# Optimization experiments

Measured on AMD Instinct MI355X. Metric: run time of the kernel, lower is better.

## Reference

```python
import jax, jax.numpy as jnp
import numpy as np
from jax import lax

H_IMG, W_IMG = 1280, 1280
STRIDES = (8, 16, 32, 64, 128)
FEAT_SHAPES = tuple((H_IMG // s) * (W_IMG // s) for s in STRIDES)  # (25600,6400,1600,400,100)
N_POINTS = sum(FEAT_SHAPES)  # 34100
NUM_CLASSES = 1
TOPK = 1000
SCORE_THRESH = 0.05
NMS_THRESH = 0.5
MAX_DET = 300
BATCH = 8
N_GT = 200


def make_points():
    # matches AnchorFreePS.reference_points: cell centers at stride*i + stride//2, (cx, cy) order
    pts = []
    for s in STRIDES:
        h, w = H_IMG // s, W_IMG // s
        cx = np.arange(w, dtype=np.float32) * s + s // 2
        cy = np.arange(h, dtype=np.float32) * s + s // 2
        gy, gx = np.meshgrid(cy, cx, indexing='ij')
        pts.append(np.stack([gx, gy], axis=-1).reshape(-1, 2))
    return jnp.asarray(np.concatenate(pts, axis=0))


def setup_inputs() -> dict:
    key = jax.random.key(0)
    k1, k2, k3, k4 = jax.random.split(key, 4)
    points = make_points()  # [N,2]
    xy = jax.random.uniform(k1, (BATCH, N_GT, 2), minval=0.0, maxval=1000.0)
    wh = jax.random.uniform(k2, (BATCH, N_GT, 2), minval=20.0, maxval=260.0)
    gt_boxes = jnp.concatenate([xy, xy + wh], axis=-1)  # [B,M,4] x1y1x2y2
    cls_logits = jax.random.normal(k3, (BATCH, N_POINTS, NUM_CLASSES)) * 1.5 - 3.0
    regression = jax.random.uniform(k4, (BATCH, N_POINTS, 4)) * 0.1  # normalized ltrb codes
    return {"points": points, "gt_boxes": gt_boxes, "cls_logits": cls_logits, "regression": regression}


def match_points_to_boxes(points, gt_boxes):
    # point-in-box test + area-cost argmin (compute_loss matched_idxs)
    px = points[None, :, None, 0]  # [1,N,1]
    py = points[None, :, None, 1]
    b = gt_boxes[:, None, :, :]    # [B,1,M,4]
    inside = (px >= b[..., 0]) & (px <= b[..., 2]) & (py >= b[..., 1]) & (py <= b[..., 3])  # [B,N,M]
    matched = jnp.any(inside, axis=-1)  # [B,N]
    areas = (gt_boxes[..., 2] - gt_boxes[..., 0]) * (gt_boxes[..., 3] - gt_boxes[..., 1])  # [B,M]
    BIG = jnp.float32(2 ** 31 - 1)  # torch.iinfo(torch.int).max
    cost = jnp.where(inside, areas[:, None, :], BIG)
    idx = jnp.argmin(cost, axis=-1)
    return jnp.where(matched, idx, -1)


def decode_boxes(rel, pts):
    # FCOSBoxCoder.decode_single with weights (1,1,1,1)
    l = rel[:, 0] * W_IMG
    t = rel[:, 1] * H_IMG
    r = rel[:, 2] * W_IMG
    b = rel[:, 3] * H_IMG
    x, y = pts[:, 0], pts[:, 1]
    return jnp.stack([x - l, y - t, x + r, y + b], axis=-1)


def clip_boxes(boxes):
    return jnp.stack([
        jnp.clip(boxes[:, 0], 0.0, W_IMG),
        jnp.clip(boxes[:, 1], 0.0, H_IMG),
        jnp.clip(boxes[:, 2], 0.0, W_IMG),
        jnp.clip(boxes[:, 3], 0.0, H_IMG)], axis=-1)


def nms(boxes, scores, labels, valid_init):
    # fixed-size sequential NMS equivalent to batched_nms (same-label suppression)
    work = lax.stop_gradient(jnp.where(valid_init, scores, -jnp.inf))

    def body(w, _):
        i = jnp.argmax(w)
        s = w[i]
        box = boxes[i]
        x1 = jnp.maximum(box[0], boxes[:, 0])
        y1 = jnp.maximum(box[1], boxes[:, 1])
        x2 = jnp.minimum(box[2], boxes[:, 2])
        y2 = jnp.minimum(box[3], boxes[:, 3])
        inter = jnp.clip(x2 - x1, 0.0) * jnp.clip(y2 - y1, 0.0)
        a1 = (box[2] - box[0]) * (box[3] - box[1])
        a2 = (boxes[:, 2] - boxes[:, 0]) * (boxes[:, 3] - boxes[:, 1])
        iou = inter / (a1 + a2 - inter + 1e-9)
        supp = (iou > NMS_THRESH) & (labels == labels[i])
        w = jnp.where(supp, -jnp.inf, w).at[i].set(-jnp.inf)
        return w, (i, s)

    _, (idxs, picked) = lax.scan(body, work, None, length=MAX_DET)
    valid = picked > -jnp.inf
    return idxs, valid


def postprocess_image(points, cls_i, reg_i):
    bx_list, sc_list, lb_list = [], [], []
    off = 0
    for size in FEAT_SHAPES:  # fixed small level loop
        sl = slice(off, off + size)
        off += size
        scores = jax.nn.sigmoid(cls_i[sl]).reshape(-1)  # [size*C]
        k = min(TOPK, size * NUM_CLASSES)
        sc, idx = lax.top_k(scores, k)
        a = idx // NUM_CLASSES
        lb = idx % NUM_CLASSES
        bx = clip_boxes(decode_boxes(reg_i[sl][a], points[sl][a]))
        bx_list.append(bx)
        sc_list.append(sc)
        lb_list.append(lb)
    boxes = jnp.concatenate(bx_list, axis=0)
    scores = jnp.concatenate(sc_list, axis=0)
    labels = jnp.concatenate(lb_list, axis=0)
    idxs, valid = nms(boxes, scores, labels, scores > SCORE_THRESH)
    out_boxes = jnp.where(valid[:, None], boxes[idxs], 0.0)
    out_scores = jnp.where(valid, scores[idxs], 0.0)
    out_labels = jnp.where(valid, labels[idxs], -1)
    return out_boxes, out_scores, out_labels, valid


def reference(points, gt_boxes, cls_logits, regression):
    matched_idxs = match_points_to_boxes(points, gt_boxes)  # [B,N]
    boxes, scores, labels, valid = jax.vmap(
        lambda c, r: postprocess_image(points, c, r))(cls_logits, regression)
    return matched_idxs, boxes, scores, labels, valid
```

## Files before the change

kernel.cpp:

```cpp
#include <hip/hip_runtime.h>
#include <stdint.h>

#define N_POINTS   34100
#define BATCH      8
#define N_GT       200
#define NLEV       5
#define NCAND      3500
#define MAX_DET    300
#define SCORE_TH   0.05f
#define NMS_TH     0.5f
#define IMG        1280.0f
#define NBIN       4096
#define TIE_CAP    4096
#define MTH 0.50000002980232238769531250

#define OUT_MATCH  0
#define OUT_BOXES  272800
#define OUT_SCORES 282400
#define OUT_LABELS 284800
#define OUT_VALID  287200

#define WS_KEYS    0
#define WS_PARAMS  1746560
#define WS_SBOX    2632192
#define WS_SSC     3080192
#define WS_MASK    3192192
#define WS_DIAG    9500032
#define MASK_STRIDE 98560
#define DIAG_STRIDE 3520

typedef unsigned long long u64;
typedef uint32_t u32;

__device__ __forceinline__ int mask_off(int c) {
    int g = c >> 6;
    return 64 * (55 * g - (g * (g - 1)) / 2) + (c - (g << 6)) * (55 - g);
}

__device__ __forceinline__ int level_of(int p) {
    return (p < 25600) ? 0 : (p < 32000) ? 1 : (p < 33600) ? 2 : (p < 34000) ? 3 : 4;
}
__device__ __forceinline__ int loff_of(int l) {
    return (l == 0) ? 0 : (l == 1) ? 25600 : (l == 2) ? 32000 : (l == 3) ? 33600 : 34000;
}
__device__ __forceinline__ int lsize_of(int l) {
    return (l == 0) ? 25600 : (l == 1) ? 6400 : (l == 2) ? 1600 : (l == 3) ? 400 : 100;
}
__device__ __forceinline__ int k_of(int l) {
    return (l == 0) ? 1000 : (l == 1) ? 1000 : (l == 2) ? 1000 : (l == 3) ? 400 : 100;
}
__device__ __forceinline__ u64 readlane64(u64 v, int t) {
    u32 lo = (u32)__builtin_amdgcn_readlane((int)(u32)v, t);
    u32 hi = (u32)__builtin_amdgcn_readlane((int)(u32)(v >> 32), t);
    return ((u64)hi << 32) | lo;
}

#define MPT 2
__global__ __launch_bounds__(256)
void match_key_kernel(const float* __restrict__ points,
                      const float* __restrict__ gt,
                      const float* __restrict__ logits,
                      float* __restrict__ out_match,
                      u32* __restrict__ keys) {
#pragma clang fp contract(off)
    __shared__ float bx1[N_GT], by1[N_GT], bx2[N_GT], by2[N_GT], ar[N_GT];
    const int b = blockIdx.y;
    const int base = blockIdx.x * (256 * MPT) + threadIdx.x;

    for (int j = threadIdx.x; j < N_GT; j += 256) {
        float x1 = gt[(b * N_GT + j) * 4 + 0];
        float y1 = gt[(b * N_GT + j) * 4 + 1];
        float x2 = gt[(b * N_GT + j) * 4 + 2];
        float y2 = gt[(b * N_GT + j) * 4 + 3];
        bx1[j] = x1; by1[j] = y1; bx2[j] = x2; by2[j] = y2;
        ar[j] = (x2 - x1) * (y2 - y1);
    }
    __syncthreads();

    const float BIGF = 2147483648.0f;
    float px[MPT], py[MPT], best[MPT];
    int bi[MPT];
#pragma unroll
    for (int k = 0; k < MPT; ++k) {
        int p = base + k * 256;
        int pc = (p < N_POINTS) ? p : 0;
        px[k] = points[pc * 2 + 0];
        py[k] = points[pc * 2 + 1];
        best[k] = BIGF; bi[k] = -1;
    }
    for (int j = 0; j < N_GT; ++j) {
        float x1 = bx1[j], y1 = by1[j], x2 = bx2[j], y2 = by2[j], a = ar[j];
#pragma unroll
        for (int k = 0; k < MPT; ++k) {
            bool inside = (px[k] >= x1) && (px[k] <= x2) &&
                          (py[k] >= y1) && (py[k] <= y2);
            float cost = inside ? a : BIGF;
            if (cost < best[k]) { best[k] = cost; bi[k] = j; }
        }
    }
#pragma unroll
    for (int k = 0; k < MPT; ++k) {
        int p = base + k * 256;
        if (p >= N_POINTS) continue;
        out_match[b * N_POINTS + p] = (float)bi[k];
        float lg = logits[b * N_POINTS + p];
        float s = 1.0f / (1.0f + expf(-lg));
        u32 u = __float_as_uint(s);
        u32 key = (u & 0x80000000u) ? ~u : (u | 0x80000000u);
        keys[b * N_POINTS + p] = key;
    }
}

__global__ __launch_bounds__(256)
void hist_select_kernel(const u32* __restrict__ keys,
                        u32* __restrict__ params) {
    __shared__ u32 h[NBIN];
    const int seg = blockIdx.x;
    const int b = seg / NLEV;
    const int l = seg - b * NLEV;
    const int tid = threadIdx.x;

    for (int i = tid; i < NBIN; i += 256) h[i] = 0u;
    __syncthreads();

    const u32* k = keys + b * N_POINTS + loff_of(l);
    const int n = lsize_of(l);
    for (int i = tid; i < n; i += 256)
        atomicAdd(&h[(k[i] >> 19) & 4095u], 1u);
    __syncthreads();

    if (tid < 64) {
        const u32 K = (u32)k_of(l);
        const int lane = tid;
        u32 S = 0;
#pragma unroll 8
        for (int i = 0; i < 64; ++i) S += h[lane * 64 + i];
        u32 acc = S;
#pragma unroll
        for (int off = 1; off < 64; off <<= 1) {
            u32 v = (u32)__shfl_down((int)acc, off);
            if (lane + off < 64) acc += v;
        }
        u32 sfxAfter = acc - S;
        bool hit = (sfxAfter < K) && (sfxAfter + S >= K);
        u64 bal = __ballot(hit);
        int Lg = (int)__builtin_ctzll(bal);
        u32 sfxG = (u32)__shfl((int)sfxAfter, Lg);

        u32 v = h[Lg * 64 + lane];
        u32 acc2 = v;
#pragma unroll
        for (int off = 1; off < 64; off <<= 1) {
            u32 t = (u32)__shfl_down((int)acc2, off);
            if (lane + off < 64) acc2 += t;
        }
        u32 sfx2 = sfxG + acc2 - v;
        bool hit2 = (sfx2 < K) && (sfx2 + v >= K);
        if (hit2) {
            params[seg * 2 + 0] = (u32)(Lg * 64 + lane);
            params[seg * 2 + 1] = K - sfx2;
        }
    }
}

#define SORT_T 1024
__global__ __launch_bounds__(SORT_T)
void pipeline_kernel(const u32* __restrict__ keys,
                     const u32* __restrict__ params,
                     const float* __restrict__ reg,
                     const float* __restrict__ points,
                     float* __restrict__ sboxes,
                     float* __restrict__ sscores) {
#pragma clang fp contract(off)
    __shared__ u64 sk[4096];
    __shared__ u64 tb[TIE_CAP];
    __shared__ u64 aux[4096];
    __shared__ u32 h[NBIN];
    __shared__ u32 bs[NBIN];
    __shared__ u32 sTl[NLEV], skkl[NLEV], wt[16];
    __shared__ u32 scnt, stcnt;

    const int b = blockIdx.x;
    const int tid = threadIdx.x;
    const int lane = tid & 63;
    const int wid = tid >> 6;
    const u32* kk_ = keys + b * N_POINTS;

    if (tid < NLEV) {
        sTl[tid]  = params[(b * NLEV + tid) * 2 + 0];
        skkl[tid] = params[(b * NLEV + tid) * 2 + 1];
    }
    if (tid == 0) { scnt = 0u; stcnt = 0u; }
    __syncthreads();

    const int NPAIR = N_POINTS / 2;
    for (int i0 = tid; i0 - tid < NPAIR; i0 += SORT_T) {
        bool act = i0 < NPAIR;
        int p0 = act ? (2 * i0) : 0;
        int p1 = p0 + 1;
        u32 key0 = kk_[p0], key1 = kk_[p1];
        int l0 = level_of(p0), l1 = level_of(p1);
        u32 d0 = (key0 >> 19) & 4095u, d1 = (key1 >> 19) & 4095u;
        u32 T0 = sTl[l0], T1 = sTl[l1];
        bool def0 = act && (d0 > T0), def1 = act && (d1 > T1);
        bool tie0 = act && (d0 == T0), tie1 = act && (d1 == T1);
        u64 k0 = ((u64)key0 << 18) | ((u64)(7 - l0) << 15)
               | (u64)(32767 - (p0 - loff_of(l0)));
        u64 k1 = ((u64)key1 << 18) | ((u64)(7 - l1) << 15)
               | (u64)(32767 - (p1 - loff_of(l1)));

        u32 nd = (u32)def0 + (u32)def1;
        u32 pre = nd;
#pragma unroll
        for (int off = 1; off < 64; off <<= 1) {
            u32 v = (u32)__shfl_up((int)pre, off);
            if (lane >= off) pre += v;
        }
        u32 base_ = 0;
        if (lane == 63 && pre) base_ = atomicAdd(&scnt, pre);
        base_ = (u32)__shfl((int)base_, 63);
        u32 ex = pre - nd;
        if (def0) sk[base_ + ex] = k0;
        if (def1) sk[base_ + ex + (u32)def0] = k1;

        u32 nt = (u32)tie0 + (u32)tie1;
        u32 pret = nt;
#pragma unroll
        for (int off = 1; off < 64; off <<= 1) {
            u32 v = (u32)__shfl_up((int)pret, off);
            if (lane >= off) pret += v;
        }
        u32 baset = 0;
        if (lane == 63 && pret) baset = atomicAdd(&stcnt, pret);
        baset = (u32)__shfl((int)baset, 63);
        u32 ext = pret - nt;
        if (tie0 && baset + ext < TIE_CAP) tb[baset + ext] = k0;
        if (tie1 && baset + ext + (u32)tie0 < TIE_CAP)
            tb[baset + ext + (u32)tie0] = k1;
    }
    __syncthreads();

    const u64 below = (lane == 0) ? 0ull : (~0ull >> (64 - lane));
    int t = (int)stcnt; if (t > TIE_CAP) t = TIE_CAP;
    for (int j0 = tid; j0 - tid < t; j0 += SORT_T) {
        bool active = j0 < t;
        u64 kj = active ? tb[j0] : 0ull;
        u32 lvtag = (u32)(kj >> 15) & 7u;
        int r = 0;
        for (int i = 0; i < t; ++i) {
            u64 ki = tb[i];
            r += (ki > kj && (((u32)(ki >> 15) & 7u) == lvtag)) ? 1 : 0;
        }
        bool inc = active && (r < (int)skkl[7 - lvtag]);
        u64 grp = __ballot(inc);
        if (grp) {
            int leader = (int)__builtin_ctzll(grp);
            u32 base_ = 0;
            if (lane == leader)
                base_ = atomicAdd(&scnt, (u32)__builtin_popcountll(grp));
            base_ = (u32)__shfl((int)base_, leader);
            if (inc) sk[base_ + (u32)__builtin_popcountll(grp & below)] = kj;
        }
    }
    __syncthreads();
    const int total = (int)scnt;

    for (int i = tid; i < NBIN; i += SORT_T) h[i] = 0u;
    __syncthreads();
    for (int i = tid; i < total; i += SORT_T)
        atomicAdd(&h[(u32)(sk[i] >> 37) & 4095u], 1u);
    __syncthreads();

    u32 t0 = h[4095 - 4 * tid];
    u32 t1 = h[4095 - (4 * tid + 1)];
    u32 t2 = h[4095 - (4 * tid + 2)];
    u32 t3 = h[4095 - (4 * tid + 3)];
    u32 tsum = t0 + t1 + t2 + t3;
    u32 sc_ = tsum;
#pragma unroll
    for (int off = 1; off < 64; off <<= 1) {
        u32 v = (u32)__shfl_up((int)sc_, off);
        if (lane >= off) sc_ += v;
    }
    if (lane == 63) wt[wid] = sc_;
    __syncthreads();
    if (tid < 64) {
        u32 v = (tid < 16) ? wt[tid] : 0u;
        u32 s2 = v;
#pragma unroll
        for (int off = 1; off < 16; off <<= 1) {
            u32 x = (u32)__shfl_up((int)s2, off);
            if (tid >= off) s2 += x;
        }
        if (tid < 16) wt[tid] = s2 - v;
    }
    __syncthreads();
    u32 run = (sc_ - tsum) + wt[wid];
    bs[4095 - 4 * tid] = run;       run += t0;
    bs[4095 - (4 * tid + 1)] = run; run += t1;
    bs[4095 - (4 * tid + 2)] = run; run += t2;
    bs[4095 - (4 * tid + 3)] = run;
    __syncthreads();
    for (int i = tid; i < NBIN; i += SORT_T) h[i] = 0u;
    __syncthreads();
    for (int i = tid; i < total; i += SORT_T) {
        u64 k = sk[i];
        u32 d = (u32)(k >> 37) & 4095u;
        u32 pos = bs[d] + atomicAdd(&h[d], 1u);
        aux[pos] = k;
    }
    __syncthreads();
    for (int p = tid; p < total; p += SORT_T) {
        u64 kp = aux[p];
        u32 d = (u32)(kp >> 37) & 4095u;
        u32 gbase = bs[d];
        u32 gend = (d == 0) ? (u32)total : bs[d - 1];
        u32 r = 0;
        for (u32 q = gbase; q < gend; ++q) r += (aux[q] > kp) ? 1u : 0u;
        sk[gbase + r] = kp;
    }
    __syncthreads();

    for (int r = tid; r < NCAND; r += SORT_T) {
        float x1 = 0.f, y1 = 0.f, x2 = 0.f, y2 = 0.f, sc = 0.f;
        if (r < total) {
            u64 k50 = sk[r];
            int lowb = (int)(k50 & 0x3FFFFull);
            int l = 7 - (lowb >> 15);
            int idxl = 32767 - (lowb & 32767);
            int p = loff_of(l) + idxl;
            u32 key32 = (u32)(k50 >> 18);
            sc = __uint_as_float(key32 ^ 0x80000000u);
            int gp = b * N_POINTS + p;
            float l_ = reg[gp * 4 + 0] * IMG;
            float t_ = reg[gp * 4 + 1] * IMG;
            float r_ = reg[gp * 4 + 2] * IMG;
            float bb = reg[gp * 4 + 3] * IMG;
            float px = points[p * 2 + 0];
            float py = points[p * 2 + 1];
            x1 = fminf(fmaxf(px - l_, 0.0f), IMG);
            y1 = fminf(fmaxf(py - t_, 0.0f), IMG);
            x2 = fminf(fmaxf(px + r_, 0.0f), IMG);
            y2 = fminf(fmaxf(py + bb, 0.0f), IMG);
        }
        int slot = b * NCAND + r;
        sboxes[slot * 4 + 0] = x1;
        sboxes[slot * 4 + 1] = y1;
        sboxes[slot * 4 + 2] = x2;
        sboxes[slot * 4 + 3] = y2;
        sscores[slot] = sc;
    }
}

__global__ __launch_bounds__(256)
void mask_kernel(const float* __restrict__ sboxes,
                 const float* __restrict__ sscores,
                 u64* __restrict__ mask,
                 u64* __restrict__ diag) {
#pragma clang fp contract(off)
    const int b = blockIdx.y;
    const int wv = threadIdx.x >> 6;
    const int lane = threadIdx.x & 63;
    const int NG = (NCAND + 3) >> 2;
    const int NH = (NG + 1) >> 1;
    const int gidx = blockIdx.x * 4 + wv;
    if (gidx >= NH) return;

    const float4* gb = (const float4*)sboxes + b * NCAND;
    const float* gs = sscores + b * NCAND;
    u64* mout = mask + (size_t)b * MASK_STRIDE;
    u64* dout = diag + (size_t)b * DIAG_STRIDE;

    for (int s = 0; s < 2; ++s) {
        const int g0 = (s == 0) ? gidx : (NG - 1 - gidx);
        if (s == 1 && g0 == gidx) break;
        const int c0 = g0 << 2;

        float4 bc[4]; float a1[4]; bool ok[4]; int g[4]; u64* rp[4];
        bool any = false;
#pragma unroll
        for (int i = 0; i < 4; ++i) {
            int c = c0 + i;
            int cc = (c < NCAND) ? c : (NCAND - 1);
            bc[i] = gb[cc];
            a1[i] = (bc[i].z - bc[i].x) * (bc[i].w - bc[i].y);
            ok[i] = (c < NCAND) && (gs[cc] > SCORE_TH);
            g[i] = cc >> 6;
            rp[i] = mout + mask_off(cc) - g[i];
            any |= ok[i];
        }
        if (!any) continue;

        for (int w = (c0 >> 6); w < 55; ++w) {
            int cj = (w << 6) + lane;
            float4 bj = (cj < NCAND) ? gb[cj] : make_float4(0.f, 0.f, 0.f, 0.f);
            float a2 = (bj.z - bj.x) * (bj.w - bj.y);
#pragma unroll
            for (int i = 0; i < 4; ++i) {
                float x1 = fmaxf(bc[i].x, bj.x);
                float y1 = fmaxf(bc[i].y, bj.y);
                float x2 = fminf(bc[i].z, bj.z);
                float y2 = fminf(bc[i].w, bj.w);
                float inter = fmaxf(x2 - x1, 0.f) * fmaxf(y2 - y1, 0.f);
                float denom = a1[i] + a2 - inter + 1e-9f;
                float hf = 0.5f * denom;
                float rr = fmaf(0x1p-25f, denom, hf);
                u64 bits = __ballot(inter > rr);
                u64 eq = __ballot(inter == rr);
                if (eq) {
                    u64 fb = __ballot((double)inter > MTH * (double)denom);
                    bits |= (eq & fb);
                }
                if (lane == 0 && ok[i] && w >= g[i]) {
                    rp[i][w] = bits;
                    if (w == g[i]) dout[c0 + i] = bits;
                }
            }
        }
    }
}

__global__ __launch_bounds__(64)
void scan_kernel(const float* __restrict__ sboxes,
                 const float* __restrict__ sscores,
                 const u64* __restrict__ mask,
                 const u64* __restrict__ diag,
                 float* __restrict__ out) {
    const int b = blockIdx.x;
    const int lane = threadIdx.x;
    const float4* gb = (const float4*)sboxes + b * NCAND;
    const float* gs = sscores + b * NCAND;
    const u64* mrow = mask + (size_t)b * MASK_STRIDE;
    const u64* drow = diag + (size_t)b * DIAG_STRIDE;

    float* ob = out + OUT_BOXES  + b * MAX_DET * 4;
    float* os = out + OUT_SCORES + b * MAX_DET;
    float* ol = out + OUT_LABELS + b * MAX_DET;
    float* ov = out + OUT_VALID  + b * MAX_DET;

    u64 m = 0ull;
    u64 rowN = drow[lane];
    float4 bjN = gb[lane];
    float sjN = gs[lane];

    int kept = 0;
    for (int w = 0; w < 55; ++w) {
        const int wbase = w << 6;
        const u64 row = rowN;
        const float4 bj = bjN;
        const float sj = sjN;
        if (w < 54) {
            int cn = wbase + 64 + lane;
            int cc = (cn < NCAND) ? cn : (NCAND - 1);
            rowN = drow[cc];
            bjN = gb[cc];
            float s = gs[cc];
            sjN = (cn < NCAND) ? s : 0.f;
        }
        int c = wbase + lane;
        u64 bad = __ballot(!((c < NCAND) && (sj > SCORE_TH)));
        u64 cur = readlane64(m, w) | bad;
        u64 km = 0ull;
        while (kept < MAX_DET) {
            u64 avail = ~cur;
            if (avail == 0ull) break;
            int t = (int)__builtin_ctzll(avail);
            u64 r = readlane64(row, t);
            cur |= r | (1ull << t);
            km |= 1ull << t;
            if (lane == t) {
                ob[kept * 4 + 0] = bj.x;
                ob[kept * 4 + 1] = bj.y;
                ob[kept * 4 + 2] = bj.z;
                ob[kept * 4 + 3] = bj.w;
                os[kept] = sj;
                ol[kept] = 0.0f;
                ov[kept] = 1.0f;
            }
            kept++;
        }
        if (km) {
            const bool lr = (lane >= w && lane < 55);
            const int lo = lane - w;
            u64 acc = 0ull;
            while (km) {
#define POPBIT(tn) int tn = -1; if (km) { tn = (int)__builtin_ctzll(km); km &= km - 1ull; }
                POPBIT(t0) POPBIT(t1) POPBIT(t2) POPBIT(t3)
                POPBIT(t4) POPBIT(t5) POPBIT(t6) POPBIT(t7)
#undef POPBIT
                u64 v0 = 0, v1 = 0, v2 = 0, v3 = 0, v4 = 0, v5 = 0, v6 = 0, v7 = 0;
                if (lr) {
                    v0 = mrow[mask_off(wbase + t0) + lo];
                    if (t1 >= 0) v1 = mrow[mask_off(wbase + t1) + lo];
                    if (t2 >= 0) v2 = mrow[mask_off(wbase + t2) + lo];
                    if (t3 >= 0) v3 = mrow[mask_off(wbase + t3) + lo];
                    if (t4 >= 0) v4 = mrow[mask_off(wbase + t4) + lo];
                    if (t5 >= 0) v5 = mrow[mask_off(wbase + t5) + lo];
                    if (t6 >= 0) v6 = mrow[mask_off(wbase + t6) + lo];
                    if (t7 >= 0) v7 = mrow[mask_off(wbase + t7) + lo];
                }
                acc |= ((v0 | v1) | (v2 | v3)) | ((v4 | v5) | (v6 | v7));
            }
            m |= acc;
        }
        if (kept >= MAX_DET) break;
    }
    for (int k = kept + lane; k < MAX_DET; k += 64) {
        ob[k * 4 + 0] = 0.f; ob[k * 4 + 1] = 0.f;
        ob[k * 4 + 2] = 0.f; ob[k * 4 + 3] = 0.f;
        os[k] = 0.f; ol[k] = -1.f; ov[k] = 0.f;
    }
}

extern "C" void kernel_launch(void* const* d_in, const int* in_sizes, int n_in,
                              void* d_out, int out_size, void* d_ws, size_t ws_size,
                              hipStream_t stream) {
    const float* points = (const float*)d_in[0];
    const float* gt     = (const float*)d_in[1];
    const float* logits = (const float*)d_in[2];
    const float* reg    = (const float*)d_in[3];
    float* out = (float*)d_out;

    u32* keys      = (u32*)((char*)d_ws + WS_KEYS);
    u32* params    = (u32*)((char*)d_ws + WS_PARAMS);
    float* sboxes  = (float*)((char*)d_ws + WS_SBOX);
    float* sscores = (float*)((char*)d_ws + WS_SSC);
    u64* mask   = (u64*)((char*)d_ws + WS_MASK);
    u64* diag   = (u64*)((char*)d_ws + WS_DIAG);

    dim3 g1((N_POINTS + 256 * MPT - 1) / (256 * MPT), BATCH);
    match_key_kernel<<<g1, 256, 0, stream>>>(points, gt, logits,
                                             out + OUT_MATCH, keys);

    hist_select_kernel<<<BATCH * NLEV, 256, 0, stream>>>(keys, params);

    pipeline_kernel<<<BATCH, SORT_T, 0, stream>>>(keys, params, reg, points,
                                                  sboxes, sscores);

    dim3 g5((((NCAND + 3) / 4 + 1) / 2 + 3) / 4, BATCH);
    mask_kernel<<<g5, 256, 0, stream>>>(sboxes, sscores, mask, diag);

    scan_kernel<<<BATCH, 64, 0, stream>>>(sboxes, sscores, mask, diag, out);
}
```

Baseline: 280.6 us.

## Fuse all stages into one cooperative persistent kernel with grid syncs

Merges the five launches (match/keys, histogram select, per-image sort/decode, mask build, NMS scan) into a single cooperative kernel of 256 blocks of 1024 threads, separated by grid-wide syncs. The point-to-box matching now runs on the spare blocks while the 8 per-image sort blocks work, so those two stages overlap. The aim is to remove launch gaps and let the large matching work hide behind the serial per-image sort. In exchange, all stages share one large static shared-memory buffer and 1024-thread blocks, which can lower occupancy. Grid syncs add their own latency, and a cooperative launch needs every block to be resident at once.

```diff
diff --git a/kernel.cpp b/kernel.cpp
--- a/kernel.cpp
+++ b/kernel.cpp
@@ -1,5 +1,8 @@
 #include <hip/hip_runtime.h>
+#include <hip/hip_cooperative_groups.h>
 #include <stdint.h>
+
+namespace cg = cooperative_groups;
 
 #define N_POINTS   34100
 #define BATCH      8
@@ -29,6 +32,9 @@
 #define MASK_STRIDE 98560
 #define DIAG_STRIDE 3520
 
+#define NBLK   256
+#define NTHR   1024
+
 typedef unsigned long long u64;
 typedef uint32_t u32;
 
@@ -36,7 +42,6 @@
     int g = c >> 6;
     return 64 * (55 * g - (g * (g - 1)) / 2) + (c - (g << 6)) * (55 - g);
 }
-
 __device__ __forceinline__ int level_of(int p) {
     return (p < 25600) ? 0 : (p < 32000) ? 1 : (p < 33600) ? 2 : (p < 34000) ? 3 : 4;
 }
@@ -55,460 +60,453 @@
     return ((u64)hi << 32) | lo;
 }
 
-#define MPT 2
-__global__ __launch_bounds__(256)
-void match_key_kernel(const float* __restrict__ points,
-                      const float* __restrict__ gt,
-                      const float* __restrict__ logits,
-                      float* __restrict__ out_match,
-                      u32* __restrict__ keys) {
+__global__ __launch_bounds__(NTHR)
+void mega_kernel(const float* __restrict__ points,
+                 const float* __restrict__ gt,
+                 const float* __restrict__ logits,
+                 const float* __restrict__ reg,
+                 float* __restrict__ out,
+                 u32* __restrict__ keys,
+                 u32* __restrict__ params,
+                 float* __restrict__ sboxes,
+                 float* __restrict__ sscores,
+                 u64* __restrict__ mask,
+                 u64* __restrict__ diag) {
 #pragma clang fp contract(off)
-    __shared__ float bx1[N_GT], by1[N_GT], bx2[N_GT], by2[N_GT], ar[N_GT];
-    const int b = blockIdx.y;
-    const int base = blockIdx.x * (256 * MPT) + threadIdx.x;
-
-    for (int j = threadIdx.x; j < N_GT; j += 256) {
-        float x1 = gt[(b * N_GT + j) * 4 + 0];
-        float y1 = gt[(b * N_GT + j) * 4 + 1];
-        float x2 = gt[(b * N_GT + j) * 4 + 2];
-        float y2 = gt[(b * N_GT + j) * 4 + 3];
-        bx1[j] = x1; by1[j] = y1; bx2[j] = x2; by2[j] = y2;
-        ar[j] = (x2 - x1) * (y2 - y1);
-    }
-    __syncthreads();
-
-    const float BIGF = 2147483648.0f;
-    float px[MPT], py[MPT], best[MPT];
-    int bi[MPT];
-#pragma unroll
-    for (int k = 0; k < MPT; ++k) {
-        int p = base + k * 256;
-        int pc = (p < N_POINTS) ? p : 0;
-        px[k] = points[pc * 2 + 0];
-        py[k] = points[pc * 2 + 1];
-        best[k] = BIGF; bi[k] = -1;
-    }
-    for (int j = 0; j < N_GT; ++j) {
-        float x1 = bx1[j], y1 = by1[j], x2 = bx2[j], y2 = by2[j], a = ar[j];
-#pragma unroll
-        for (int k = 0; k < MPT; ++k) {
-            bool inside = (px[k] >= x1) && (px[k] <= x2) &&
-                          (py[k] >= y1) && (py[k] <= y2);
-            float cost = inside ? a : BIGF;
-            if (cost < best[k]) { best[k] = cost; bi[k] = j; }
-        }
-    }
-#pragma unroll
-    for (int k = 0; k < MPT; ++k) {
-        int p = base + k * 256;
-        if (p >= N_POINTS) continue;
-        out_match[b * N_POINTS + p] = (float)bi[k];
-        float lg = logits[b * N_POINTS + p];
-        float s = 1.0f / (1.0f + expf(-lg));
-        u32 u = __float_as_uint(s);
-        u32 key = (u & 0x80000000u) ? ~u : (u | 0x80000000u);
-        keys[b * N_POINTS + p] = key;
-    }
-}
-
-__global__ __launch_bounds__(256)
-void hist_select_kernel(const u32* __restrict__ keys,
-                        u32* __restrict__ params) {
-    __shared__ u32 h[NBIN];
-    const int seg = blockIdx.x;
-    const int b = seg / NLEV;
-    const int l = seg - b * NLEV;
-    const int tid = threadIdx.x;
-
-    for (int i = tid; i < NBIN; i += 256) h[i] = 0u;
-    __syncthreads();
-
-    const u32* k = keys + b * N_POINTS + loff_of(l);
-    const int n = lsize_of(l);
-    for (int i = tid; i < n; i += 256)
-        atomicAdd(&h[(k[i] >> 19) & 4095u], 1u);
-    __syncthreads();
-
-    if (tid < 64) {
-        const u32 K = (u32)k_of(l);
-        const int lane = tid;
-        u32 S = 0;
-#pragma unroll 8
-        for (int i = 0; i < 64; ++i) S += h[lane * 64 + i];
-        u32 acc = S;
-#pragma unroll
-        for (int off = 1; off < 64; off <<= 1) {
-            u32 v = (u32)__shfl_down((int)acc, off);
-            if (lane + off < 64) acc += v;
-        }
-        u32 sfxAfter = acc - S;
-        bool hit = (sfxAfter < K) && (sfxAfter + S >= K);
-        u64 bal = __ballot(hit);
-        int Lg = (int)__builtin_ctzll(bal);
-        u32 sfxG = (u32)__shfl((int)sfxAfter, Lg);
-
-        u32 v = h[Lg * 64 + lane];
-        u32 acc2 = v;
-#pragma unroll
-        for (int off = 1; off < 64; off <<= 1) {
-            u32 t = (u32)__shfl_down((int)acc2, off);
-            if (lane + off < 64) acc2 += t;
-        }
-        u32 sfx2 = sfxG + acc2 - v;
-        bool hit2 = (sfx2 < K) && (sfx2 + v >= K);
-        if (hit2) {
-            params[seg * 2 + 0] = (u32)(Lg * 64 + lane);
-            params[seg * 2 + 1] = K - sfx2;
-        }
-    }
-}
-
-#define SORT_T 1024
-__global__ __launch_bounds__(SORT_T)
-void pipeline_kernel(const u32* __restrict__ keys,
-                     const u32* __restrict__ params,
-                     const float* __restrict__ reg,
-                     const float* __restrict__ points,
-                     float* __restrict__ sboxes,
-                     float* __restrict__ sscores) {
-#pragma clang fp contract(off)
-    __shared__ u64 sk[4096];
-    __shared__ u64 tb[TIE_CAP];
-    __shared__ u64 aux[4096];
-    __shared__ u32 h[NBIN];
-    __shared__ u32 bs[NBIN];
+    cg::grid_group gg = cg::this_grid();
+    __shared__ __align__(16) char smem[131072];
     __shared__ u32 sTl[NLEV], skkl[NLEV], wt[16];
     __shared__ u32 scnt, stcnt;
 
-    const int b = blockIdx.x;
     const int tid = threadIdx.x;
     const int lane = tid & 63;
     const int wid = tid >> 6;
-    const u32* kk_ = keys + b * N_POINTS;
-
-    if (tid < NLEV) {
-        sTl[tid]  = params[(b * NLEV + tid) * 2 + 0];
-        skkl[tid] = params[(b * NLEV + tid) * 2 + 1];
+    const int blk = blockIdx.x;
+
+    for (int i = blk * NTHR + tid; i < BATCH * N_POINTS; i += NBLK * NTHR) {
+        float lgv = logits[i];
+        float s = 1.0f / (1.0f + expf(-lgv));
+        u32 u = __float_as_uint(s);
+        keys[i] = (u & 0x80000000u) ? ~u : (u | 0x80000000u);
     }
-    if (tid == 0) { scnt = 0u; stcnt = 0u; }
-    __syncthreads();
-
-    const int NPAIR = N_POINTS / 2;
-    for (int i0 = tid; i0 - tid < NPAIR; i0 += SORT_T) {
-        bool act = i0 < NPAIR;
-        int p0 = act ? (2 * i0) : 0;
-        int p1 = p0 + 1;
-        u32 key0 = kk_[p0], key1 = kk_[p1];
-        int l0 = level_of(p0), l1 = level_of(p1);
-        u32 d0 = (key0 >> 19) & 4095u, d1 = (key1 >> 19) & 4095u;
-        u32 T0 = sTl[l0], T1 = sTl[l1];
-        bool def0 = act && (d0 > T0), def1 = act && (d1 > T1);
-        bool tie0 = act && (d0 == T0), tie1 = act && (d1 == T1);
-        u64 k0 = ((u64)key0 << 18) | ((u64)(7 - l0) << 15)
-               | (u64)(32767 - (p0 - loff_of(l0)));
-        u64 k1 = ((u64)key1 << 18) | ((u64)(7 - l1) << 15)
-               | (u64)(32767 - (p1 - loff_of(l1)));
-
-        u32 nd = (u32)def0 + (u32)def1;
-        u32 pre = nd;
+    gg.sync();
+
+    if (blk < BATCH * NLEV) {
+        u32* h2 = (u32*)smem;
+        const int seg = blk;
+        const int b = seg / NLEV;
+        const int l = seg - b * NLEV;
+        for (int i = tid; i < NBIN; i += NTHR) h2[i] = 0u;
+        __syncthreads();
+        const u32* k = keys + b * N_POINTS + loff_of(l);
+        const int n = lsize_of(l);
+        for (int i = tid; i < n; i += NTHR)
+            atomicAdd(&h2[(k[i] >> 19) & 4095u], 1u);
+        __syncthreads();
+        if (tid < 64) {
+            const u32 K = (u32)k_of(l);
+            u32 S = 0;
+#pragma unroll 8
+            for (int i = 0; i < 64; ++i) S += h2[lane * 64 + i];
+            u32 acc = S;
+#pragma unroll
+            for (int off = 1; off < 64; off <<= 1) {
+                u32 v = (u32)__shfl_down((int)acc, off);
+                if (lane + off < 64) acc += v;
+            }
+            u32 sfxAfter = acc - S;
+            bool hit = (sfxAfter < K) && (sfxAfter + S >= K);
+            u64 bal = __ballot(hit);
+            int Lg = (int)__builtin_ctzll(bal);
+            u32 sfxG = (u32)__shfl((int)sfxAfter, Lg);
+            u32 v = h2[Lg * 64 + lane];
+            u32 acc2 = v;
+#pragma unroll
+            for (int off = 1; off < 64; off <<= 1) {
+                u32 t = (u32)__shfl_down((int)acc2, off);
+                if (lane + off < 64) acc2 += t;
+            }
+            u32 sfx2 = sfxG + acc2 - v;
+            bool hit2 = (sfx2 < K) && (sfx2 + v >= K);
+            if (hit2) {
+                params[seg * 2 + 0] = (u32)(Lg * 64 + lane);
+                params[seg * 2 + 1] = K - sfx2;
+            }
+        }
+    }
+    gg.sync();
+
+    if (blk < BATCH) {
+        u64* sk  = (u64*)smem;
+        u64* tb  = (u64*)(smem + 32768);
+        u64* aux = (u64*)(smem + 65536);
+        u32* h   = (u32*)(smem + 98304);
+        u32* bs  = (u32*)(smem + 114688);
+        const int b = blk;
+        const u32* kk_ = keys + b * N_POINTS;
+
+        if (tid < NLEV) {
+            sTl[tid]  = params[(b * NLEV + tid) * 2 + 0];
+            skkl[tid] = params[(b * NLEV + tid) * 2 + 1];
+        }
+        if (tid == 0) { scnt = 0u; stcnt = 0u; }
+        __syncthreads();
+
+        const int NPAIR = N_POINTS / 2;
+        for (int i0 = tid; i0 - tid < NPAIR; i0 += NTHR) {
+            bool act = i0 < NPAIR;
+            int p0 = act ? (2 * i0) : 0;
+            int p1 = p0 + 1;
+            u32 key0 = kk_[p0], key1 = kk_[p1];
+            int l0 = level_of(p0), l1 = level_of(p1);
+            u32 d0 = (key0 >> 19) & 4095u, d1 = (key1 >> 19) & 4095u;
+            u32 T0 = sTl[l0], T1 = sTl[l1];
+            bool def0 = act && (d0 > T0), def1 = act && (d1 > T1);
+            bool tie0 = act && (d0 == T0), tie1 = act && (d1 == T1);
+            u64 k0 = ((u64)key0 << 18) | ((u64)(7 - l0) << 15)
+                   | (u64)(32767 - (p0 - loff_of(l0)));
+            u64 k1 = ((u64)key1 << 18) | ((u64)(7 - l1) << 15)
+                   | (u64)(32767 - (p1 - loff_of(l1)));
+
+            u32 nd = (u32)def0 + (u32)def1;
+            u32 pre = nd;
+#pragma unroll
+            for (int off = 1; off < 64; off <<= 1) {
+                u32 v = (u32)__shfl_up((int)pre, off);
+                if (lane >= off) pre += v;
+            }
+            u32 base_ = 0;
+            if (lane == 63 && pre) base_ = atomicAdd(&scnt, pre);
+            base_ = (u32)__shfl((int)base_, 63);
+            u32 ex = pre - nd;
+            if (def0) sk[base_ + ex] = k0;
+            if (def1) sk[base_ + ex + (u32)def0] = k1;
+
+            u32 nt = (u32)tie0 + (u32)tie1;
+            u32 pret = nt;
+#pragma unroll
+            for (int off = 1; off < 64; off <<= 1) {
+                u32 v = (u32)__shfl_up((int)pret, off);
+                if (lane >= off) pret += v;
+            }
+            u32 baset = 0;
+            if (lane == 63 && pret) baset = atomicAdd(&stcnt, pret);
+            baset = (u32)__shfl((int)baset, 63);
+            u32 ext = pret - nt;
+            if (tie0 && baset + ext < TIE_CAP) tb[baset + ext] = k0;
+            if (tie1 && baset + ext + (u32)tie0 < TIE_CAP)
+                tb[baset + ext + (u32)tie0] = k1;
+        }
+        __syncthreads();
+
+        const u64 below = (lane == 0) ? 0ull : (~0ull >> (64 - lane));
+        int t = (int)stcnt; if (t > TIE_CAP) t = TIE_CAP;
+        for (int j0 = tid; j0 - tid < t; j0 += NTHR) {
+            bool active = j0 < t;
+            u64 kj = active ? tb[j0] : 0ull;
+            u32 lvtag = (u32)(kj >> 15) & 7u;
+            int r = 0;
+            for (int i = 0; i < t; ++i) {
+                u64 ki = tb[i];
+                r += (ki > kj && (((u32)(ki >> 15) & 7u) == lvtag)) ? 1 : 0;
+            }
+            bool inc = active && (r < (int)skkl[7 - lvtag]);
+            u64 grp = __ballot(inc);
+            if (grp) {
+                int leader = (int)__builtin_ctzll(grp);
+                u32 base_ = 0;
+                if (lane == leader)
+                    base_ = atomicAdd(&scnt, (u32)__builtin_popcountll(grp));
+                base_ = (u32)__shfl((int)base_, leader);
+                if (inc) sk[base_ + (u32)__builtin_popcountll(grp & below)] = kj;
+            }
+        }
+        __syncthreads();
+        const int total = (int)scnt;
+
+        for (int i = tid; i < NBIN; i += NTHR) h[i] = 0u;
+        __syncthreads();
+        for (int i = tid; i < total; i += NTHR)
+            atomicAdd(&h[(u32)(sk[i] >> 37) & 4095u], 1u);
+        __syncthreads();
+
+        u32 t0 = h[4095 - 4 * tid];
+        u32 t1 = h[4095 - (4 * tid + 1)];
+        u32 t2 = h[4095 - (4 * tid + 2)];
+        u32 t3 = h[4095 - (4 * tid + 3)];
+        u32 tsum = t0 + t1 + t2 + t3;
+        u32 sc_ = tsum;
 #pragma unroll
         for (int off = 1; off < 64; off <<= 1) {
-            u32 v = (u32)__shfl_up((int)pre, off);
-            if (lane >= off) pre += v;
-        }
-        u32 base_ = 0;
-        if (lane == 63 && pre) base_ = atomicAdd(&scnt, pre);
-        base_ = (u32)__shfl((int)base_, 63);
-        u32 ex = pre - nd;
-        if (def0) sk[base_ + ex] = k0;
-        if (def1) sk[base_ + ex + (u32)def0] = k1;
-
-        u32 nt = (u32)tie0 + (u32)tie1;
-        u32 pret = nt;
-#pragma unroll
-        for (int off = 1; off < 64; off <<= 1) {
-            u32 v = (u32)__shfl_up((int)pret, off);
-            if (lane >= off) pret += v;
-        }
-        u32 baset = 0;
-        if (lane == 63 && pret) baset = atomicAdd(&stcnt, pret);
-        baset = (u32)__shfl((int)baset, 63);
-        u32 ext = pret - nt;
-        if (tie0 && baset + ext < TIE_CAP) tb[baset + ext] = k0;
-        if (tie1 && baset + ext + (u32)tie0 < TIE_CAP)
-            tb[baset + ext + (u32)tie0] = k1;
+            u32 v = (u32)__shfl_up((int)sc_, off);
+            if (lane >= off) sc_ += v;
+        }
+        if (lane == 63) wt[wid] = sc_;
+        __syncthreads();
+        if (tid < 64) {
+            u32 v = (tid < 16) ? wt[tid] : 0u;
+            u32 s2 = v;
+#pragma unroll
+            for (int off = 1; off < 16; off <<= 1) {
+                u32 x = (u32)__shfl_up((int)s2, off);
+                if (tid >= off) s2 += x;
+            }
+            if (tid < 16) wt[tid] = s2 - v;
+        }
+        __syncthreads();
+        u32 run = (sc_ - tsum) + wt[wid];
+        bs[4095 - 4 * tid] = run;       run += t0;
+        bs[4095 - (4 * tid + 1)] = run; run += t1;
+        bs[4095 - (4 * tid + 2)] = run; run += t2;
+        bs[4095 - (4 * tid + 3)] = run;
+        __syncthreads();
+        for (int i = tid; i < NBIN; i += NTHR) h[i] = 0u;
+        __syncthreads();
+        for (int i = tid; i < total; i += NTHR) {
+            u64 k = sk[i];
+            u32 d = (u32)(k >> 37) & 4095u;
+            u32 pos = bs[d] + atomicAdd(&h[d], 1u);
+            aux[pos] = k;
+        }
+        __syncthreads();
+        for (int p = tid; p < total; p += NTHR) {
+            u64 kp = aux[p];
+            u32 d = (u32)(kp >> 37) & 4095u;
+            u32 gbase = bs[d];
+            u32 gend = (d == 0) ? (u32)total : bs[d - 1];
+            u32 r = 0;
+            for (u32 q = gbase; q < gend; ++q) r += (aux[q] > kp) ? 1u : 0u;
+            sk[gbase + r] = kp;
+        }
+        __syncthreads();
+
+        for (int r = tid; r < NCAND; r += NTHR) {
+            float x1 = 0.f, y1 = 0.f, x2 = 0.f, y2 = 0.f, sc = 0.f;
+            if (r < total) {
+                u64 k50 = sk[r];
+                int lowb = (int)(k50 & 0x3FFFFull);
+                int l = 7 - (lowb >> 15);
+                int idxl = 32767 - (lowb & 32767);
+                int p = loff_of(l) + idxl;
+                u32 key32 = (u32)(k50 >> 18);
+                sc = __uint_as_float(key32 ^ 0x80000000u);
+                int gp = b * N_POINTS + p;
+                float l_ = reg[gp * 4 + 0] * IMG;
+                float t_ = reg[gp * 4 + 1] * IMG;
+                float r_ = reg[gp * 4 + 2] * IMG;
+                float bb = reg[gp * 4 + 3] * IMG;
+                float px = points[p * 2 + 0];
+                float py = points[p * 2 + 1];
+                x1 = fminf(fmaxf(px - l_, 0.0f), IMG);
+                y1 = fminf(fmaxf(py - t_, 0.0f), IMG);
+                x2 = fminf(fmaxf(px + r_, 0.0f), IMG);
+                y2 = fminf(fmaxf(py + bb, 0.0f), IMG);
+            }
+            int slot = b * NCAND + r;
+            sboxes[slot * 4 + 0] = x1;
+            sboxes[slot * 4 + 1] = y1;
+            sboxes[slot * 4 + 2] = x2;
+            sboxes[slot * 4 + 3] = y2;
+            sscores[slot] = sc;
+        }
+    } else {
+        float* bx1 = (float*)smem;
+        float* by1 = bx1 + 256;
+        float* bx2 = bx1 + 512;
+        float* by2 = bx1 + 768;
+        float* ar  = bx1 + 1024;
+        const int q = blk - BATCH;
+        const int b = q / 31;
+        const int j = q - b * 31;
+        for (int i = tid; i < N_GT; i += NTHR) {
+            float x1 = gt[(b * N_GT + i) * 4 + 0];
+            float y1 = gt[(b * N_GT + i) * 4 + 1];
+            float x2 = gt[(b * N_GT + i) * 4 + 2];
+            float y2 = gt[(b * N_GT + i) * 4 + 3];
+            bx1[i] = x1; by1[i] = y1; bx2[i] = x2; by2[i] = y2;
+            ar[i] = (x2 - x1) * (y2 - y1);
+        }
+        __syncthreads();
+
+        const float BIGF = 2147483648.0f;
+        const int STR = 31 * NTHR;
+        float px[2], py[2], best[2];
+        int bi[2];
+#pragma unroll
+        for (int k = 0; k < 2; ++k) {
+            int p = j * NTHR + tid + k * STR;
+            int pc = (p < N_POINTS) ? p : 0;
+            px[k] = points[pc * 2 + 0];
+            py[k] = points[pc * 2 + 1];
+            best[k] = BIGF; bi[k] = -1;
+        }
+        for (int i = 0; i < N_GT; ++i) {
+            float x1 = bx1[i], y1 = by1[i], x2 = bx2[i], y2 = by2[i], a = ar[i];
+#pragma unroll
+            for (int k = 0; k < 2; ++k) {
+                bool inside = (px[k] >= x1) && (px[k] <= x2) &&
+                              (py[k] >= y1) && (py[k] <= y2);
+                float cost = inside ? a : BIGF;
+                if (cost < best[k]) { best[k] = cost; bi[k] = i; }
+            }
+        }
+#pragma unroll
+        for (int k = 0; k < 2; ++k) {
+            int p = j * NTHR + tid + k * STR;
+            if (p < N_POINTS)
+                out[OUT_MATCH + b * N_POINTS + p] = (float)bi[k];
+        }
     }
-    __syncthreads();
-
-    const u64 below = (lane == 0) ? 0ull : (~0ull >> (64 - lane));
-    int t = (int)stcnt; if (t > TIE_CAP) t = TIE_CAP;
-    for (int j0 = tid; j0 - tid < t; j0 += SORT_T) {
-        bool active = j0 < t;
-        u64 kj = active ? tb[j0] : 0ull;
-        u32 lvtag = (u32)(kj >> 15) & 7u;
-        int r = 0;
-        for (int i = 0; i < t; ++i) {
-            u64 ki = tb[i];
-            r += (ki > kj && (((u32)(ki >> 15) & 7u) == lvtag)) ? 1 : 0;
-        }
-        bool inc = active && (r < (int)skkl[7 - lvtag]);
-        u64 grp = __ballot(inc);
-        if (grp) {
-            int leader = (int)__builtin_ctzll(grp);
-            u32 base_ = 0;
-            if (lane == leader)
-                base_ = atomicAdd(&scnt, (u32)__builtin_popcountll(grp));
-            base_ = (u32)__shfl((int)base_, leader);
-            if (inc) sk[base_ + (u32)__builtin_popcountll(grp & below)] = kj;
+    gg.sync();
+
+    {
+        const int NG = (NCAND + 3) >> 2;
+        const int NH = (NG + 1) >> 1;
+        const int wg = blk * 16 + wid;
+        if (wg < NH * BATCH) {
+            const int b = wg & 7;
+            const int gidx = wg >> 3;
+            const float4* gb = (const float4*)sboxes + b * NCAND;
+            const float* gs = sscores + b * NCAND;
+            u64* mout = mask + (size_t)b * MASK_STRIDE;
+            u64* dout = diag + (size_t)b * DIAG_STRIDE;
+
+            for (int s = 0; s < 2; ++s) {
+                const int g0 = (s == 0) ? gidx : (NG - 1 - gidx);
+                if (s == 1 && g0 == gidx) break;
+                const int c0 = g0 << 2;
+
+                float4 bc[4]; float a1[4]; bool ok[4]; int g[4]; u64* rp[4];
+                bool any = false;
+#pragma unroll
+                for (int i = 0; i < 4; ++i) {
+                    int c = c0 + i;
+                    int cc = (c < NCAND) ? c : (NCAND - 1);
+                    bc[i] = gb[cc];
+                    a1[i] = (bc[i].z - bc[i].x) * (bc[i].w - bc[i].y);
+                    ok[i] = (c < NCAND) && (gs[cc] > SCORE_TH);
+                    g[i] = cc >> 6;
+                    rp[i] = mout + mask_off(cc) - g[i];
+                    any |= ok[i];
+                }
+                if (!any) continue;
+
+                for (int w = (c0 >> 6); w < 55; ++w) {
+                    int cj = (w << 6) + lane;
+                    float4 bj = (cj < NCAND) ? gb[cj]
+                                             : make_float4(0.f, 0.f, 0.f, 0.f);
+                    float a2 = (bj.z - bj.x) * (bj.w - bj.y);
+#pragma unroll
+                    for (int i = 0; i < 4; ++i) {
+                        float x1 = fmaxf(bc[i].x, bj.x);
+                        float y1 = fmaxf(bc[i].y, bj.y);
+                        float x2 = fminf(bc[i].z, bj.z);
+                        float y2 = fminf(bc[i].w, bj.w);
+                        float inter = fmaxf(x2 - x1, 0.f) * fmaxf(y2 - y1, 0.f);
+                        float denom = a1[i] + a2 - inter + 1e-9f;
+                        float hf = 0.5f * denom;
+                        float rr = fmaf(0x1p-25f, denom, hf);
+                        u64 bits = __ballot(inter > rr);
+                        u64 eq = __ballot(inter == rr);
+                        if (eq) {
+                            u64 fb = __ballot((double)inter > MTH * (double)denom);
+                            bits |= (eq & fb);
+                        }
+                        if (lane == 0 && ok[i] && w >= g[i]) {
+                            rp[i][w] = bits;
+                            if (w == g[i]) dout[c0 + i] = bits;
+                        }
+                    }
+                }
+            }
         }
     }
-    __syncthreads();
-    const int total = (int)scnt;
-
-    for (int i = tid; i < NBIN; i += SORT_T) h[i] = 0u;
-    __syncthreads();
-    for (int i = tid; i < total; i += SORT_T)
-        atomicAdd(&h[(u32)(sk[i] >> 37) & 4095u], 1u);
-    __syncthreads();
-
-    u32 t0 = h[4095 - 4 * tid];
-    u32 t1 = h[4095 - (4 * tid + 1)];
-    u32 t2 = h[4095 - (4 * tid + 2)];
-    u32 t3 = h[4095 - (4 * tid + 3)];
-    u32 tsum = t0 + t1 + t2 + t3;
-    u32 sc_ = tsum;
-#pragma unroll
-    for (int off = 1; off < 64; off <<= 1) {
-        u32 v = (u32)__shfl_up((int)sc_, off);
-        if (lane >= off) sc_ += v;
-    }
-    if (lane == 63) wt[wid] = sc_;
-    __syncthreads();
-    if (tid < 64) {
-        u32 v = (tid < 16) ? wt[tid] : 0u;
-        u32 s2 = v;
-#pragma unroll
-        for (int off = 1; off < 16; off <<= 1) {
-            u32 x = (u32)__shfl_up((int)s2, off);
-            if (tid >= off) s2 += x;
-        }
-        if (tid < 16) wt[tid] = s2 - v;
-    }
-    __syncthreads();
-    u32 run = (sc_ - tsum) + wt[wid];
-    bs[4095 - 4 * tid] = run;       run += t0;
-    bs[4095 - (4 * tid + 1)] = run; run += t1;
-    bs[4095 - (4 * tid + 2)] = run; run += t2;
-    bs[4095 - (4 * tid + 3)] = run;
-    __syncthreads();
-    for (int i = tid; i < NBIN; i += SORT_T) h[i] = 0u;
-    __syncthreads();
-    for (int i = tid; i < total; i += SORT_T) {
-        u64 k = sk[i];
-        u32 d = (u32)(k >> 37) & 4095u;
-        u32 pos = bs[d] + atomicAdd(&h[d], 1u);
-        aux[pos] = k;
-    }
-    __syncthreads();
-    for (int p = tid; p < total; p += SORT_T) {
-        u64 kp = aux[p];
-        u32 d = (u32)(kp >> 37) & 4095u;
-        u32 gbase = bs[d];
-        u32 gend = (d == 0) ? (u32)total : bs[d - 1];
-        u32 r = 0;
-        for (u32 q = gbase; q < gend; ++q) r += (aux[q] > kp) ? 1u : 0u;
-        sk[gbase + r] = kp;
-    }
-    __syncthreads();
-
-    for (int r = tid; r < NCAND; r += SORT_T) {
-        float x1 = 0.f, y1 = 0.f, x2 = 0.f, y2 = 0.f, sc = 0.f;
-        if (r < total) {
-            u64 k50 = sk[r];
-            int lowb = (int)(k50 & 0x3FFFFull);
-            int l = 7 - (lowb >> 15);
-            int idxl = 32767 - (lowb & 32767);
-            int p = loff_of(l) + idxl;
-            u32 key32 = (u32)(k50 >> 18);
-            sc = __uint_as_float(key32 ^ 0x80000000u);
-            int gp = b * N_POINTS + p;
-            float l_ = reg[gp * 4 + 0] * IMG;
-            float t_ = reg[gp * 4 + 1] * IMG;
-            float r_ = reg[gp * 4 + 2] * IMG;
-            float bb = reg[gp * 4 + 3] * IMG;
-            float px = points[p * 2 + 0];
-            float py = points[p * 2 + 1];
-            x1 = fminf(fmaxf(px - l_, 0.0f), IMG);
-            y1 = fminf(fmaxf(py - t_, 0.0f), IMG);
-            x2 = fminf(fmaxf(px + r_, 0.0f), IMG);
-            y2 = fminf(fmaxf(py + bb, 0.0f), IMG);
-        }
-        int slot = b * NCAND + r;
-        sboxes[slot * 4 + 0] = x1;
-        sboxes[slot * 4 + 1] = y1;
-        sboxes[slot * 4 + 2] = x2;
-        sboxes[slot * 4 + 3] = y2;
-        sscores[slot] = sc;
-    }
-}
-
-__global__ __launch_bounds__(256)
-void mask_kernel(const float* __restrict__ sboxes,
-                 const float* __restrict__ sscores,
-                 u64* __restrict__ mask,
-                 u64* __restrict__ diag) {
-#pragma clang fp contract(off)
-    const int b = blockIdx.y;
-    const int wv = threadIdx.x >> 6;
-    const int lane = threadIdx.x & 63;
-    const int NG = (NCAND + 3) >> 2;
-    const int NH = (NG + 1) >> 1;
-    const int gidx = blockIdx.x * 4 + wv;
-    if (gidx >= NH) return;
-
-    const float4* gb = (const float4*)sboxes + b * NCAND;
-    const float* gs = sscores + b * NCAND;
-    u64* mout = mask + (size_t)b * MASK_STRIDE;
-    u64* dout = diag + (size_t)b * DIAG_STRIDE;
-
-    for (int s = 0; s < 2; ++s) {
-        const int g0 = (s == 0) ? gidx : (NG - 1 - gidx);
-        if (s == 1 && g0 == gidx) break;
-        const int c0 = g0 << 2;
-
-        float4 bc[4]; float a1[4]; bool ok[4]; int g[4]; u64* rp[4];
-        bool any = false;
-#pragma unroll
-        for (int i = 0; i < 4; ++i) {
-            int c = c0 + i;
-            int cc = (c < NCAND) ? c : (NCAND - 1);
-            bc[i] = gb[cc];
-            a1[i] = (bc[i].z - bc[i].x) * (bc[i].w - bc[i].y);
-            ok[i] = (c < NCAND) && (gs[cc] > SCORE_TH);
-            g[i] = cc >> 6;
-            rp[i] = mout + mask_off(cc) - g[i];
-            any |= ok[i];
-        }
-        if (!any) continue;
-
-        for (int w = (c0 >> 6); w < 55; ++w) {
-            int cj = (w << 6) + lane;
-            float4 bj = (cj < NCAND) ? gb[cj] : make_float4(0.f, 0.f, 0.f, 0.f);
-            float a2 = (bj.z - bj.x) * (bj.w - bj.y);
-#pragma unroll
-            for (int i = 0; i < 4; ++i) {
-                float x1 = fmaxf(bc[i].x, bj.x);
-                float y1 = fmaxf(bc[i].y, bj.y);
-                float x2 = fminf(bc[i].z, bj.z);
-                float y2 = fminf(bc[i].w, bj.w);
-                float inter = fmaxf(x2 - x1, 0.f) * fmaxf(y2 - y1, 0.f);
-                float denom = a1[i] + a2 - inter + 1e-9f;
-                float hf = 0.5f * denom;
-                float rr = fmaf(0x1p-25f, denom, hf);
-                u64 bits = __ballot(inter > rr);
-                u64 eq = __ballot(inter == rr);
-                if (eq) {
-                    u64 fb = __ballot((double)inter > MTH * (double)denom);
-                    bits |= (eq & fb);
+    gg.sync();
+
+    if (blk < BATCH && tid < 64) {
+        const int b = blk;
+        const float4* gb = (const float4*)sboxes + b * NCAND;
+        const float* gs = sscores + b * NCAND;
+        const u64* mrow = mask + (size_t)b * MASK_STRIDE;
+        const u64* drow = diag + (size_t)b * DIAG_STRIDE;
+
+        float* ob = out + OUT_BOXES  + b * MAX_DET * 4;
+        float* os = out + OUT_SCORES + b * MAX_DET;
+        float* ol = out + OUT_LABELS + b * MAX_DET;
+        float* ov = out + OUT_VALID  + b * MAX_DET;
+
+        u64 m = 0ull;
+        u64 rowN = drow[lane];
+        float4 bjN = gb[lane];
+        float sjN = gs[lane];
+
+        int kept = 0;
+        for (int w = 0; w < 55; ++w) {
+            const int wbase = w << 6;
+            const u64 row = rowN;
+            const float4 bj = bjN;
+            const float sj = sjN;
+            if (w < 54) {
+                int cn = wbase + 64 + lane;
+                int cc = (cn < NCAND) ? cn : (NCAND - 1);
+                rowN = drow[cc];
+                bjN = gb[cc];
+                float s = gs[cc];
+                sjN = (cn < NCAND) ? s : 0.f;
+            }
+            int c = wbase + lane;
+            u64 bad = __ballot(!((c < NCAND) && (sj > SCORE_TH)));
+            u64 cur = readlane64(m, w) | bad;
+            u64 km = 0ull;
+            while (kept < MAX_DET) {
+                u64 avail = ~cur;
+                if (avail == 0ull) break;
+                int t = (int)__builtin_ctzll(avail);
+                u64 r = readlane64(row, t);
+                cur |= r | (1ull << t);
+                km |= 1ull << t;
+                if (lane == t) {
+                    ob[kept * 4 + 0] = bj.x;
+                    ob[kept * 4 + 1] = bj.y;
+                    ob[kept * 4 + 2] = bj.z;
+                    ob[kept * 4 + 3] = bj.w;
+                    os[kept] = sj;
+                    ol[kept] = 0.0f;
+                    ov[kept] = 1.0f;
                 }
-                if (lane == 0 && ok[i] && w >= g[i]) {
-                    rp[i][w] = bits;
-                    if (w == g[i]) dout[c0 + i] = bits;
+                kept++;
+            }
+            if (km) {
+                const bool lr = (lane >= w && lane < 55);
+                const int lo = lane - w;
+                u64 acc = 0ull;
+                while (km) {
+#define POPBIT(tn) int tn = -1; if (km) { tn = (int)__builtin_ctzll(km); km &= km - 1ull; }
+                    POPBIT(t0) POPBIT(t1) POPBIT(t2) POPBIT(t3)
+                    POPBIT(t4) POPBIT(t5) POPBIT(t6) POPBIT(t7)
+#undef POPBIT
+                    u64 v0 = 0, v1 = 0, v2 = 0, v3 = 0, v4 = 0, v5 = 0, v6 = 0, v7 = 0;
+                    if (lr) {
+                        v0 = mrow[mask_off(wbase + t0) + lo];
+                        if (t1 >= 0) v1 = mrow[mask_off(wbase + t1) + lo];
+                        if (t2 >= 0) v2 = mrow[mask_off(wbase + t2) + lo];
+                        if (t3 >= 0) v3 = mrow[mask_off(wbase + t3) + lo];
+                        if (t4 >= 0) v4 = mrow[mask_off(wbase + t4) + lo];
+                        if (t5 >= 0) v5 = mrow[mask_off(wbase + t5) + lo];
+                        if (t6 >= 0) v6 = mrow[mask_off(wbase + t6) + lo];
+                        if (t7 >= 0) v7 = mrow[mask_off(wbase + t7) + lo];
+                    }
+                    acc |= ((v0 | v1) | (v2 | v3)) | ((v4 | v5) | (v6 | v7));
                 }
-            }
-        }
-    }
-}
-
-__global__ __launch_bounds__(64)
-void scan_kernel(const float* __restrict__ sboxes,
-                 const float* __restrict__ sscores,
-                 const u64* __restrict__ mask,
-                 const u64* __restrict__ diag,
-                 float* __restrict__ out) {
-    const int b = blockIdx.x;
-    const int lane = threadIdx.x;
-    const float4* gb = (const float4*)sboxes + b * NCAND;
-    const float* gs = sscores + b * NCAND;
-    const u64* mrow = mask + (size_t)b * MASK_STRIDE;
-    const u64* drow = diag + (size_t)b * DIAG_STRIDE;
-
-    float* ob = out + OUT_BOXES  + b * MAX_DET * 4;
-    float* os = out + OUT_SCORES + b * MAX_DET;
-    float* ol = out + OUT_LABELS + b * MAX_DET;
-    float* ov = out + OUT_VALID  + b * MAX_DET;
-
-    u64 m = 0ull;
-    u64 rowN = drow[lane];
-    float4 bjN = gb[lane];
-    float sjN = gs[lane];
-
-    int kept = 0;
-    for (int w = 0; w < 55; ++w) {
-        const int wbase = w << 6;
-        const u64 row = rowN;
-        const float4 bj = bjN;
-        const float sj = sjN;
-        if (w < 54) {
-            int cn = wbase + 64 + lane;
-            int cc = (cn < NCAND) ? cn : (NCAND - 1);
-            rowN = drow[cc];
-            bjN = gb[cc];
-            float s = gs[cc];
-            sjN = (cn < NCAND) ? s : 0.f;
-        }
-        int c = wbase + lane;
-        u64 bad = __ballot(!((c < NCAND) && (sj > SCORE_TH)));
-        u64 cur = readlane64(m, w) | bad;
-        u64 km = 0ull;
-        while (kept < MAX_DET) {
-            u64 avail = ~cur;
-            if (avail == 0ull) break;
-            int t = (int)__builtin_ctzll(avail);
-            u64 r = readlane64(row, t);
-            cur |= r | (1ull << t);
-            km |= 1ull << t;
-            if (lane == t) {
-                ob[kept * 4 + 0] = bj.x;
-                ob[kept * 4 + 1] = bj.y;
-                ob[kept * 4 + 2] = bj.z;
-                ob[kept * 4 + 3] = bj.w;
-                os[kept] = sj;
-                ol[kept] = 0.0f;
-                ov[kept] = 1.0f;
-            }
-            kept++;
-        }
-        if (km) {
-            const bool lr = (lane >= w && lane < 55);
-            const int lo = lane - w;
-            u64 acc = 0ull;
-            while (km) {
-#define POPBIT(tn) int tn = -1; if (km) { tn = (int)__builtin_ctzll(km); km &= km - 1ull; }
-                POPBIT(t0) POPBIT(t1) POPBIT(t2) POPBIT(t3)
-                POPBIT(t4) POPBIT(t5) POPBIT(t6) POPBIT(t7)
-#undef POPBIT
-                u64 v0 = 0, v1 = 0, v2 = 0, v3 = 0, v4 = 0, v5 = 0, v6 = 0, v7 = 0;
-                if (lr) {
-                    v0 = mrow[mask_off(wbase + t0) + lo];
-                    if (t1 >= 0) v1 = mrow[mask_off(wbase + t1) + lo];
-                    if (t2 >= 0) v2 = mrow[mask_off(wbase + t2) + lo];
-                    if (t3 >= 0) v3 = mrow[mask_off(wbase + t3) + lo];
-                    if (t4 >= 0) v4 = mrow[mask_off(wbase + t4) + lo];
-                    if (t5 >= 0) v5 = mrow[mask_off(wbase + t5) + lo];
-                    if (t6 >= 0) v6 = mrow[mask_off(wbase + t6) + lo];
-                    if (t7 >= 0) v7 = mrow[mask_off(wbase + t7) + lo];
-                }
-                acc |= ((v0 | v1) | (v2 | v3)) | ((v4 | v5) | (v6 | v7));
-            }
-            m |= acc;
-        }
-        if (kept >= MAX_DET) break;
-    }
-    for (int k = kept + lane; k < MAX_DET; k += 64) {
-        ob[k * 4 + 0] = 0.f; ob[k * 4 + 1] = 0.f;
-        ob[k * 4 + 2] = 0.f; ob[k * 4 + 3] = 0.f;
-        os[k] = 0.f; ol[k] = -1.f; ov[k] = 0.f;
+                m |= acc;
+            }
+            if (kept >= MAX_DET) break;
+        }
+        for (int k = kept + lane; k < MAX_DET; k += 64) {
+            ob[k * 4 + 0] = 0.f; ob[k * 4 + 1] = 0.f;
+            ob[k * 4 + 2] = 0.f; ob[k * 4 + 3] = 0.f;
+            os[k] = 0.f; ol[k] = -1.f; ov[k] = 0.f;
+        }
     }
 }
 
@@ -528,17 +526,11 @@
     u64* mask   = (u64*)((char*)d_ws + WS_MASK);
     u64* diag   = (u64*)((char*)d_ws + WS_DIAG);
 
-    dim3 g1((N_POINTS + 256 * MPT - 1) / (256 * MPT), BATCH);
-    match_key_kernel<<<g1, 256, 0, stream>>>(points, gt, logits,
-                                             out + OUT_MATCH, keys);
-
-    hist_select_kernel<<<BATCH * NLEV, 256, 0, stream>>>(keys, params);
-
-    pipeline_kernel<<<BATCH, SORT_T, 0, stream>>>(keys, params, reg, points,
-                                                  sboxes, sscores);
-
-    dim3 g5((((NCAND + 3) / 4 + 1) / 2 + 3) / 4, BATCH);
-    mask_kernel<<<g5, 256, 0, stream>>>(sboxes, sscores, mask, diag);
-
-    scan_kernel<<<BATCH, 64, 0, stream>>>(sboxes, sscores, mask, diag, out);
-}
+    void* args[] = {
+        (void*)&points, (void*)&gt, (void*)&logits, (void*)&reg, (void*)&out,
+        (void*)&keys, (void*)&params, (void*)&sboxes, (void*)&sscores,
+        (void*)&mask, (void*)&diag
+    };
+    hipLaunchCooperativeKernel((const void*)mega_kernel,
+                               dim3(NBLK), dim3(NTHR), args, 0, stream);
+}
```

Result: slower. 325.7 us (+16.1%).
